# Kernel optimization log

Measured on AMD Instinct MI355X. Metric: run time of the kernel, lower is better.

The kernel has to match this reference:

```python
import jax, jax.numpy as jnp
import numpy as np

N = 10000          # nodes
E = 640000         # edges (avg degree 64)
D_EMB = 32
D_FEAT = 8
D = 256            # node_encoding
LAYERS = 3         # graph_layers
FLOW_ITERS = 10
COST_C = 1.0       # square cost: c*x^2, inv_derivative(y) = y/(2c)


def setup_inputs() -> dict:
    key = jax.random.key(0)
    ks = jax.random.split(key, 20)

    def gn(k, shape):
        return jax.random.normal(k, shape, jnp.float32) / np.sqrt(shape[0]).astype(np.float32)

    return dict(
        node_features=jax.random.normal(ks[0], (N, D_FEAT), jnp.float32),
        node_embeddings=jax.random.normal(ks[1], (N, D_EMB), jnp.float32),
        demands=jax.random.normal(ks[2], (N, 1), jnp.float32),
        edge_src=jnp.sort(jax.random.randint(ks[3], (E,), 0, N, jnp.int32)),
        edge_dst=jax.random.randint(ks[4], (E,), 0, N, jnp.int32),
        W_enc=gn(ks[5], (D_EMB + D_FEAT, D)), b_enc=jnp.zeros((D,), jnp.float32),
        W_agg_in=gn(ks[6], (D, D)), W_agg_out=gn(ks[7], (D, D)), b_agg=jnp.zeros((D,), jnp.float32),
        W_z=gn(ks[8], (D, D)), U_z=gn(ks[9], (D, D)), b_z=jnp.zeros((D,), jnp.float32),
        W_r=gn(ks[10], (D, D)), U_r=gn(ks[11], (D, D)), b_r=jnp.zeros((D,), jnp.float32),
        W_h=gn(ks[12], (D, D)), U_h=gn(ks[13], (D, D)), b_h=jnp.zeros((D,), jnp.float32),
        W_dec=gn(ks[14], (D, N)), b_dec=jnp.zeros((N,), jnp.float32),
        W_d1=gn(ks[15], (D, D)), b_d1=jnp.zeros((D,), jnp.float32),
        W_d2=gn(ks[16], (D, 1)), b_d2=jnp.zeros((1,), jnp.float32),
    )


def _segment_softmax(vals, seg, num):
    # tf.sparse.softmax: softmax over the nonzero entries of each row
    m = jax.ops.segment_max(vals, seg, num_segments=num, indices_are_sorted=True)
    e = jnp.exp(vals - m[seg])
    s = jax.ops.segment_sum(e, seg, num_segments=num, indices_are_sorted=True)
    return e / s[seg]


def reference(node_features, node_embeddings, demands, edge_src, edge_dst,
              W_enc, b_enc, W_agg_in, W_agg_out, b_agg,
              W_z, U_z, b_z, W_r, U_r, b_r, W_h, U_h, b_h,
              W_dec, b_dec, W_d1, b_d1, W_d2, b_d2):
    n = node_features.shape[0]
    # node encoder (MLP, no hidden, relu)
    h = jax.nn.relu(jnp.concatenate([node_embeddings, node_features], axis=1) @ W_enc + b_enc)
    # graph layers: sparse neighborhood aggregation + GRU state update
    for _ in range(LAYERS):
        t = h @ W_agg_in                                   # [N, D]
        agg = jax.ops.segment_sum(t[edge_dst], edge_src,    # gather neighbors, scatter-add by row
                                  num_segments=n, indices_are_sorted=True)
        nxt = jnp.tanh(agg @ W_agg_out + b_agg)
        z = jax.nn.sigmoid(nxt @ W_z + h @ U_z + b_z)
        r = jax.nn.sigmoid(nxt @ W_r + h @ U_r + b_r)
        cand = jnp.tanh(nxt @ W_h + (r * h) @ U_h + b_h)
        h = z * h + (1.0 - z) * cand
    # decoder -> dense [N, N] edge weights, masked by adjacency, sparse row softmax
    pred = h @ W_dec + b_dec                                # [N, N]
    logits = pred[edge_src, edge_dst]                       # [E]
    w = _segment_softmax(logits, edge_src, n)               # flow_weight_pred values
    # sparse min-cost-flow: proportional flow iterations
    d = demands[:, 0]
    flow = jnp.zeros_like(w)
    for _ in range(FLOW_ITERS):
        inflow = jax.ops.segment_sum(flow, edge_dst, num_segments=n)
        adj_in = jax.nn.relu(inflow - d)                    # flow available to push out of each node
        flow = w * adj_in[edge_src]
    flow_cost = jnp.sum(COST_C * flow * flow)
    # dual decoder (hidden [D] relu, linear head)
    dual = jax.nn.relu(h @ W_d1 + b_d1) @ W_d2 + b_d2       # [N, 1]
    dv = dual[:, 0]
    dual_diff = dv[edge_src] - dv[edge_dst]                 # (dual_i - dual_j) on edges only
    dual_flows = jax.nn.relu(dual_diff / (2.0 * COST_C))    # relu(inv_derivative)
    dual_cost = jnp.sum(COST_C * dual_flows * dual_flows - dual_flows * dual_diff) - jnp.sum(dv * d)
    loss = flow_cost - dual_cost
    return loss, flow
```

## Files before the change

### kernel.cpp

```cpp
#include <hip/hip_runtime.h>
#include <hip/hip_bf16.h>
#include <math.h>

#define N_NODES 10000
#define N_EDGES 640000
#define DDIM 256
#define NBLK_E 2500

typedef long long i64;

__device__ __forceinline__ float sigmoidf_(float x) { return 1.0f / (1.0f + expf(-x)); }

__global__ __launch_bounds__(256) void encode_kernel(
    const float* __restrict__ feat, const float* __restrict__ emb,
    const float* __restrict__ W, const float* __restrict__ b, float* __restrict__ h)
{
    const int n = blockIdx.x;
    const int t = threadIdx.x;
    __shared__ float in_s[40];
    if (t < 32) in_s[t] = emb[(i64)n * 32 + t];
    else if (t < 40) in_s[t] = feat[(i64)n * 8 + (t - 32)];
    __syncthreads();
    float acc = b[t];
#pragma unroll
    for (int k = 0; k < 40; ++k) acc += in_s[k] * W[k * DDIM + t];
    h[(i64)n * DDIM + t] = fmaxf(acc, 0.0f);
}

enum { EPI_NONE = 0, EPI_TANH, EPI_SIGM, EPI_RH, EPI_HOUT, EPI_RELU };

template<int EPI, bool DUAL>
__global__ __launch_bounds__(256) void gemm_epi(
    const float* __restrict__ A1, const float* __restrict__ W1,
    const float* __restrict__ A2, const float* __restrict__ W2,
    const float* __restrict__ bias,
    const float* __restrict__ haux, const float* __restrict__ zaux,
    float* __restrict__ C)
{
    __shared__ __align__(16) float As[16][68];
    __shared__ __align__(16) float Bs[16][64];
    const int tid = threadIdx.x;
    const int tx = tid & 15;
    const int ty = tid >> 4;
    const int brow = blockIdx.x * 64;
    const int bcol = blockIdx.y * 64;

    const int lrow = tid >> 2;
    const int lk4  = (tid & 3) << 2;
    const int wkrow = tid >> 4;
    const int wcol4 = (tid & 15) << 2;

    const int arow = brow + lrow;
    const bool arow_ok = (arow < N_NODES);
    const i64 aoff = (i64)(arow_ok ? arow : 0) * DDIM;

    float acc[4][4] = {{0.f,0.f,0.f,0.f},{0.f,0.f,0.f,0.f},{0.f,0.f,0.f,0.f},{0.f,0.f,0.f,0.f}};

    for (int pass = 0; pass < (DUAL ? 2 : 1); ++pass) {
        const float* Ap = (pass ? A2 : A1) + aoff;
        const float* Wp = (pass ? W2 : W1);
        for (int k0 = 0; k0 < DDIM; k0 += 16) {
            float4 av = arow_ok ? *(const float4*)(Ap + k0 + lk4) : make_float4(0.f,0.f,0.f,0.f);
            float4 wv = *(const float4*)(Wp + (i64)(k0 + wkrow) * DDIM + bcol + wcol4);
            __syncthreads();
            As[lk4+0][lrow] = av.x; As[lk4+1][lrow] = av.y;
            As[lk4+2][lrow] = av.z; As[lk4+3][lrow] = av.w;
            *(float4*)&Bs[wkrow][wcol4] = wv;
            __syncthreads();
#pragma unroll
            for (int k = 0; k < 16; ++k) {
                float4 a = *(const float4*)&As[k][ty << 2];
                float4 b = *(const float4*)&Bs[k][tx << 2];
                acc[0][0] += a.x*b.x; acc[0][1] += a.x*b.y; acc[0][2] += a.x*b.z; acc[0][3] += a.x*b.w;
                acc[1][0] += a.y*b.x; acc[1][1] += a.y*b.y; acc[1][2] += a.y*b.z; acc[1][3] += a.y*b.w;
                acc[2][0] += a.z*b.x; acc[2][1] += a.z*b.y; acc[2][2] += a.z*b.z; acc[2][3] += a.z*b.w;
                acc[3][0] += a.w*b.x; acc[3][1] += a.w*b.y; acc[3][2] += a.w*b.z; acc[3][3] += a.w*b.w;
            }
        }
    }

#pragma unroll
    for (int i = 0; i < 4; ++i) {
        const int r = brow + (ty << 2) + i;
        if (r < N_NODES) {
#pragma unroll
            for (int j = 0; j < 4; ++j) {
                const int c = bcol + (tx << 2) + j;
                const i64 idx = (i64)r * DDIM + c;
                float v = acc[i][j];
                float out;
                if constexpr (EPI == EPI_NONE)      out = v;
                else if constexpr (EPI == EPI_TANH) out = tanhf(v + bias[c]);
                else if constexpr (EPI == EPI_SIGM) out = sigmoidf_(v + bias[c]);
                else if constexpr (EPI == EPI_RH)   out = sigmoidf_(v + bias[c]) * haux[idx];
                else if constexpr (EPI == EPI_HOUT) {
                    float cand = tanhf(v + bias[c]);
                    float zz = zaux[idx];
                    out = zz * haux[idx] + (1.0f - zz) * cand;
                } else                               out = fmaxf(v + bias[c], 0.0f);
                C[idx] = out;
            }
        }
    }
}

__global__ __launch_bounds__(256) void agg_kernel(
    const float* __restrict__ t, const int* __restrict__ dst, const int* __restrict__ rp,
    float* __restrict__ agg)
{
    const int n = blockIdx.x;
    const int d = threadIdx.x;
    const int s = rp[n], e = rp[n + 1];
    float a0 = 0.f, a1 = 0.f, a2 = 0.f, a3 = 0.f;
    int i = s;
    for (; i + 4 <= e; i += 4) {
        int d0 = dst[i], d1 = dst[i+1], d2 = dst[i+2], d3 = dst[i+3];
        a0 += t[(i64)d0 * DDIM + d];
        a1 += t[(i64)d1 * DDIM + d];
        a2 += t[(i64)d2 * DDIM + d];
        a3 += t[(i64)d3 * DDIM + d];
    }
    for (; i < e; ++i) a0 += t[(i64)dst[i] * DDIM + d];
    agg[(i64)n * DDIM + d] = (a0 + a1) + (a2 + a3);
}

__global__ __launch_bounds__(256) void transpose_kernel(
    const float* __restrict__ Wd, float* __restrict__ wdt)
{
    __shared__ float tile[32][33];
    const int bx = blockIdx.x;
    const int by = blockIdx.y;
    const int tx = threadIdx.x & 31, ty = threadIdx.x >> 5;
#pragma unroll
    for (int j = 0; j < 4; ++j) {
        int k = by * 32 + ty + j * 8;
        int nc = bx * 32 + tx;
        if (nc < N_NODES) tile[ty + j * 8][tx] = Wd[(i64)k * N_NODES + nc];
    }
    __syncthreads();
#pragma unroll
    for (int j = 0; j < 4; ++j) {
        int nr = bx * 32 + ty + j * 8;
        int k = by * 32 + tx;
        if (nr < N_NODES) wdt[(i64)nr * DDIM + k] = tile[tx][ty + j * 8];
    }
}

__global__ __launch_bounds__(256) void logits_softmax_kernel(
    const float* __restrict__ h, const float* __restrict__ wdt,
    const float* __restrict__ b_dec, const int* __restrict__ dst,
    const int* __restrict__ rp, float* __restrict__ w)
{
    const int n = blockIdx.x;
    const int s = rp[n], e = rp[n + 1];
    const int tid = threadIdx.x;
    const int lane = tid & 63, wv = tid >> 6;
    __shared__ __align__(16) float hs[256];
    __shared__ float sred[8];
    hs[tid] = h[(i64)n * DDIM + tid];
    __syncthreads();
    float4 hv = ((const float4*)hs)[lane];
    for (int i = s + wv; i < e; i += 4) {
        const int dd = dst[i];
        float4 a = *(const float4*)(wdt + (i64)dd * DDIM + (lane << 2));
        float p = a.x*hv.x + a.y*hv.y + a.z*hv.z + a.w*hv.w;
#pragma unroll
        for (int o = 32; o; o >>= 1) p += __shfl_down(p, o);
        if (lane == 0) w[i] = p + b_dec[dd];
    }
    __syncthreads();
    if (e <= s) return;
    float m = -INFINITY;
    for (int i = s + tid; i < e; i += 256) m = fmaxf(m, w[i]);
#pragma unroll
    for (int o = 32; o; o >>= 1) m = fmaxf(m, __shfl_down(m, o));
    if (lane == 0) sred[wv] = m;
    __syncthreads();
    m = fmaxf(fmaxf(sred[0], sred[1]), fmaxf(sred[2], sred[3]));
    float ss = 0.f;
    for (int i = s + tid; i < e; i += 256) { float ev = expf(w[i] - m); w[i] = ev; ss += ev; }
#pragma unroll
    for (int o = 32; o; o >>= 1) ss += __shfl_down(ss, o);
    if (lane == 0) sred[4 + wv] = ss;
    __syncthreads();
    ss = (sred[4] + sred[5]) + (sred[6] + sred[7]);
    float inv = 1.0f / ss;
    for (int i = s + tid; i < e; i += 256) w[i] *= inv;
}

__global__ void zero_misc_kernel(int* __restrict__ cnt, float* __restrict__ red) {
    int i = blockIdx.x * 256 + threadIdx.x;
    if (i < N_NODES) cnt[i] = 0;
    if (i < 8) red[i] = 0.0f;
}

__global__ void rowptr_kernel(const int* __restrict__ key, int* __restrict__ rp) {
    int n = blockIdx.x * 256 + threadIdx.x;
    if (n > N_NODES) return;
    int lo = 0, hi = N_EDGES;
    while (lo < hi) { int mid = (lo + hi) >> 1; if (key[mid] < n) lo = mid + 1; else hi = mid; }
    rp[n] = lo;
}

__global__ void hist_kernel(const int* __restrict__ dst, int* __restrict__ cnt) {
    int e = blockIdx.x * 256 + threadIdx.x;
    atomicAdd(&cnt[dst[e]], 1);
}

__global__ __launch_bounds__(256) void scan_kernel(int* __restrict__ cnt, int* __restrict__ rp) {
    __shared__ int part[256];
    const int t = threadIdx.x;
    const int chunk = (N_NODES + 255) / 256;
    int b = t * chunk, en = min(b + chunk, N_NODES);
    int s = 0;
    for (int i = b; i < en; ++i) s += cnt[i];
    part[t] = s;
    __syncthreads();
    for (int o = 1; o < 256; o <<= 1) {
        int v = (t >= o) ? part[t - o] : 0;
        __syncthreads();
        part[t] += v;
        __syncthreads();
    }
    int base = (t == 0) ? 0 : part[t - 1];
    for (int i = b; i < en; ++i) { rp[i] = base; base += cnt[i]; cnt[i] = 0; }
    if (t == 255) rp[N_NODES] = part[255];
}

__global__ void scatter_kernel(const int* __restrict__ src, const int* __restrict__ dst,
                               const float* __restrict__ w, const int* __restrict__ rp_d,
                               int* __restrict__ cnt, int* __restrict__ sp, float* __restrict__ wp)
{
    int e = blockIdx.x * 256 + threadIdx.x;
    int dd = dst[e];
    int pos = rp_d[dd] + atomicAdd(&cnt[dd], 1);
    sp[pos] = src[e];
    wp[pos] = w[e];
}

__global__ void init_adj_kernel(const float* __restrict__ dem, float* __restrict__ adjA) {
    int n = blockIdx.x * 256 + threadIdx.x;
    if (n < N_NODES) adjA[n] = fmaxf(-dem[n], 0.0f);
}

__global__ __launch_bounds__(256) void flow_iter_kernel(
    const float* __restrict__ wp, const int* __restrict__ sp, const int* __restrict__ rp_d,
    const float* __restrict__ adj_old, const float* __restrict__ dem, float* __restrict__ adj_new)
{
    const int n = blockIdx.x * 4 + (threadIdx.x >> 6);
    if (n >= N_NODES) return;
    const int lane = threadIdx.x & 63;
    const int s = rp_d[n], e = rp_d[n + 1];
    float acc = 0.f;
    for (int i = s + lane; i < e; i += 64) acc += wp[i] * adj_old[sp[i]];
#pragma unroll
    for (int o = 32; o; o >>= 1) acc += __shfl_down(acc, o);
    if (lane == 0) adj_new[n] = fmaxf(acc - dem[n], 0.0f);
}

__global__ __launch_bounds__(256) void flow_out_kernel(
    const float* __restrict__ w, const int* __restrict__ src, const float* __restrict__ adj,
    float* __restrict__ out_flow, float* __restrict__ red)
{
    __shared__ float sred[4];
    int e = blockIdx.x * 256 + threadIdx.x;
    float f = w[e] * adj[src[e]];
    out_flow[e] = f;
    float p = f * f;
#pragma unroll
    for (int o = 32; o; o >>= 1) p += __shfl_down(p, o);
    int lane = threadIdx.x & 63, wv = threadIdx.x >> 6;
    if (lane == 0) sred[wv] = p;
    __syncthreads();
    if (threadIdx.x == 0) atomicAdd(&red[0], (sred[0] + sred[1]) + (sred[2] + sred[3]));
}

__global__ __launch_bounds__(256) void dv_kernel(
    const float* __restrict__ t2, const float* __restrict__ Wd2, const float* __restrict__ bd2,
    const float* __restrict__ dem, float* __restrict__ dv, float* __restrict__ red)
{
    __shared__ float sred[4];
    const int n = blockIdx.x * 4 + (threadIdx.x >> 6);
    const int lane = threadIdx.x & 63, wv = threadIdx.x >> 6;
    float contrib = 0.0f;
    if (n < N_NODES) {
        float4 a = *(const float4*)(t2 + (i64)n * DDIM + (lane << 2));
        float4 b = *(const float4*)(Wd2 + (lane << 2));
        float p = a.x*b.x + a.y*b.y + a.z*b.z + a.w*b.w;
#pragma unroll
        for (int o = 32; o; o >>= 1) p += __shfl_down(p, o);
        if (lane == 0) {
            float v = p + bd2[0];
            dv[n] = v;
            contrib = v * dem[n];
        }
    }
    if (lane == 0) sred[wv] = contrib;
    __syncthreads();
    if (threadIdx.x == 0) atomicAdd(&red[2], (sred[0] + sred[1]) + (sred[2] + sred[3]));
}

__global__ __launch_bounds__(256) void dual_edge_kernel(
    const float* __restrict__ dv, const int* __restrict__ src, const int* __restrict__ dst,
    float* __restrict__ red)
{
    __shared__ float sred[4];
    int e = blockIdx.x * 256 + threadIdx.x;
    float df = dv[src[e]] - dv[dst[e]];
    float f = fmaxf(df * 0.5f, 0.0f);
    float val = f * f - f * df;
#pragma unroll
    for (int o = 32; o; o >>= 1) val += __shfl_down(val, o);
    int lane = threadIdx.x & 63, wv = threadIdx.x >> 6;
    if (lane == 0) sred[wv] = val;
    __syncthreads();
    if (threadIdx.x == 0) atomicAdd(&red[1], (sred[0] + sred[1]) + (sred[2] + sred[3]));
}

__global__ void finalize_kernel(const float* __restrict__ red, float* __restrict__ out) {
    out[0] = red[0] - red[1] + red[2];
}

extern "C" void kernel_launch(void* const* d_in, const int* in_sizes, int n_in,
                              void* d_out, int out_size, void* d_ws, size_t ws_size,
                              hipStream_t stream) {
    (void)in_sizes; (void)n_in; (void)out_size; (void)ws_size;
    const float* feat   = (const float*)d_in[0];
    const float* emb    = (const float*)d_in[1];
    const float* dem    = (const float*)d_in[2];
    const int*   e_src  = (const int*)d_in[3];
    const int*   e_dst  = (const int*)d_in[4];
    const float* W_enc  = (const float*)d_in[5];
    const float* b_enc  = (const float*)d_in[6];
    const float* W_ai   = (const float*)d_in[7];
    const float* W_ao   = (const float*)d_in[8];
    const float* b_agg  = (const float*)d_in[9];
    const float* W_z    = (const float*)d_in[10];
    const float* U_z    = (const float*)d_in[11];
    const float* b_z    = (const float*)d_in[12];
    const float* W_r    = (const float*)d_in[13];
    const float* U_r    = (const float*)d_in[14];
    const float* b_r    = (const float*)d_in[15];
    const float* W_h    = (const float*)d_in[16];
    const float* U_h    = (const float*)d_in[17];
    const float* b_h    = (const float*)d_in[18];
    const float* W_dec  = (const float*)d_in[19];
    const float* b_dec  = (const float*)d_in[20];
    const float* W_d1   = (const float*)d_in[21];
    const float* b_d1   = (const float*)d_in[22];
    const float* W_d2   = (const float*)d_in[23];
    const float* b_d2   = (const float*)d_in[24];

    float* ws = (float*)d_ws;
    const size_t F = (size_t)N_NODES * DDIM;
    float* h    = ws;
    float* t    = ws + F;
    float* agg  = ws + 2 * F;
    float* nxt  = ws + 3 * F;
    float* wbuf = ws + 4 * F;
    float* wp   = wbuf + N_EDGES;
    int*   sp   = (int*)(wp + N_EDGES);
    float* adjA = (float*)(sp + N_EDGES);
    float* adjB = adjA + N_NODES;
    float* dv   = adjB + N_NODES;
    int*   rp_s = (int*)(dv + N_NODES);
    int*   rp_d = rp_s + (N_NODES + 1);
    int*   cnt  = rp_d + (N_NODES + 1);
    float* red  = (float*)(cnt + N_NODES);
    float* zb = t;
    float* rh = agg;
    float* wdt = agg;

    const dim3 g_gemm(157, 4);

    zero_misc_kernel<<<40, 256, 0, stream>>>(cnt, red);
    encode_kernel<<<N_NODES, 256, 0, stream>>>(feat, emb, W_enc, b_enc, h);
    rowptr_kernel<<<40, 256, 0, stream>>>(e_src, rp_s);

    for (int L = 0; L < 3; ++L) {
        gemm_epi<EPI_NONE, false><<<g_gemm, 256, 0, stream>>>(h, W_ai, nullptr, nullptr, nullptr, nullptr, nullptr, t);
        agg_kernel<<<N_NODES, 256, 0, stream>>>(t, e_dst, rp_s, agg);
        gemm_epi<EPI_TANH, false><<<g_gemm, 256, 0, stream>>>(agg, W_ao, nullptr, nullptr, b_agg, nullptr, nullptr, nxt);
        gemm_epi<EPI_SIGM, true><<<g_gemm, 256, 0, stream>>>(nxt, W_z, h, U_z, b_z, nullptr, nullptr, zb);
        gemm_epi<EPI_RH, true><<<g_gemm, 256, 0, stream>>>(nxt, W_r, h, U_r, b_r, h, nullptr, rh);
        gemm_epi<EPI_HOUT, true><<<g_gemm, 256, 0, stream>>>(nxt, W_h, rh, U_h, b_h, h, zb, h);
    }

    transpose_kernel<<<dim3(313, 8), 256, 0, stream>>>(W_dec, wdt);
    logits_softmax_kernel<<<N_NODES, 256, 0, stream>>>(h, wdt, b_dec, e_dst, rp_s, wbuf);

    hist_kernel<<<NBLK_E, 256, 0, stream>>>(e_dst, cnt);
    scan_kernel<<<1, 256, 0, stream>>>(cnt, rp_d);
    scatter_kernel<<<NBLK_E, 256, 0, stream>>>(e_src, e_dst, wbuf, rp_d, cnt, sp, wp);

    init_adj_kernel<<<40, 256, 0, stream>>>(dem, adjA);
    float* aold = adjA; float* anew = adjB;
    for (int it = 0; it < 9; ++it) {
        flow_iter_kernel<<<2500, 256, 0, stream>>>(wp, sp, rp_d, aold, dem, anew);
        float* tmp = aold; aold = anew; anew = tmp;
    }
    flow_out_kernel<<<NBLK_E, 256, 0, stream>>>(wbuf, e_src, aold, (float*)d_out + 1, red);

    gemm_epi<EPI_RELU, false><<<g_gemm, 256, 0, stream>>>(h, W_d1, nullptr, nullptr, b_d1, nullptr, nullptr, t);
    dv_kernel<<<2500, 256, 0, stream>>>(t, W_d2, b_d2, dem, dv, red);
    dual_edge_kernel<<<NBLK_E, 256, 0, stream>>>(dv, e_src, e_dst, red);
    finalize_kernel<<<1, 1, 0, stream>>>(red, (float*)d_out);
}
```

Baseline: 1.389 ms.

## Replace fp32 SIMT GEMMs with split-bf16 MFMA GEMMs for dense layers

```diff
diff --git a/kernel.cpp b/kernel.cpp
--- a/kernel.cpp
+++ b/kernel.cpp
@@ -8,8 +8,19 @@
 #define NBLK_E 2500
 
 typedef long long i64;
+typedef __attribute__((ext_vector_type(8))) short short8;
+typedef __attribute__((ext_vector_type(4))) float f32x4;
 
 __device__ __forceinline__ float sigmoidf_(float x) { return 1.0f / (1.0f + expf(-x)); }
+__device__ __forceinline__ short bf16_hi(float f, float& hf) {
+    __hip_bfloat16 h = __float2bfloat16(f);
+    hf = __bfloat162float(h);
+    return __builtin_bit_cast(short, h);
+}
+__device__ __forceinline__ short bf16_of(float f) {
+    __hip_bfloat16 h = __float2bfloat16(f);
+    return __builtin_bit_cast(short, h);
+}
 
 __global__ __launch_bounds__(256) void encode_kernel(
     const float* __restrict__ feat, const float* __restrict__ emb,
@@ -27,78 +38,120 @@
     h[(i64)n * DDIM + t] = fmaxf(acc, 0.0f);
 }
 
+struct Wsrc { const float* s[9]; };
+
+__global__ __launch_bounds__(256) void conv_w_kernel(Wsrc wsrc, short* __restrict__ wt)
+{
+    const int m = blockIdx.y;
+    const float* __restrict__ src = wsrc.s[m];
+    short* dh = wt + (i64)m * 131072;
+    short* dl = dh + 65536;
+    const int e = blockIdx.x * 256 + threadIdx.x;
+    const int c = e >> 8, k = e & 255;
+    const float f = src[k * 256 + c];
+    float hf;
+    const short hb = bf16_hi(f, hf);
+    dh[(i64)c * 256 + k] = hb;
+    dl[(i64)c * 256 + k] = bf16_of(f - hf);
+}
+
 enum { EPI_NONE = 0, EPI_TANH, EPI_SIGM, EPI_RH, EPI_HOUT, EPI_RELU };
 
+__device__ __forceinline__ void load_cvt_frag(const float* __restrict__ p, bool ok,
+                                              short8& hi, short8& lo)
+{
+    f32x4 v0 = {}, v1 = {};
+    if (ok) { v0 = *(const f32x4*)p; v1 = *(const f32x4*)(p + 4); }
+#pragma unroll
+    for (int j = 0; j < 4; ++j) {
+        float h0f, h1f;
+        hi[j]     = bf16_hi(v0[j], h0f);
+        hi[j + 4] = bf16_hi(v1[j], h1f);
+        lo[j]     = bf16_of(v0[j] - h0f);
+        lo[j + 4] = bf16_of(v1[j] - h1f);
+    }
+}
+
 template<int EPI, bool DUAL>
-__global__ __launch_bounds__(256) void gemm_epi(
-    const float* __restrict__ A1, const float* __restrict__ W1,
-    const float* __restrict__ A2, const float* __restrict__ W2,
+__global__ __launch_bounds__(256) void gemm_mfma(
+    const float* __restrict__ A1, const short* __restrict__ W1h, const short* __restrict__ W1l,
+    const float* __restrict__ A2, const short* __restrict__ W2h, const short* __restrict__ W2l,
     const float* __restrict__ bias,
     const float* __restrict__ haux, const float* __restrict__ zaux,
     float* __restrict__ C)
 {
-    __shared__ __align__(16) float As[16][68];
-    __shared__ __align__(16) float Bs[16][64];
     const int tid = threadIdx.x;
-    const int tx = tid & 15;
-    const int ty = tid >> 4;
-    const int brow = blockIdx.x * 64;
-    const int bcol = blockIdx.y * 64;
-
-    const int lrow = tid >> 2;
-    const int lk4  = (tid & 3) << 2;
-    const int wkrow = tid >> 4;
-    const int wcol4 = (tid & 15) << 2;
-
-    const int arow = brow + lrow;
-    const bool arow_ok = (arow < N_NODES);
-    const i64 aoff = (i64)(arow_ok ? arow : 0) * DDIM;
-
-    float acc[4][4] = {{0.f,0.f,0.f,0.f},{0.f,0.f,0.f,0.f},{0.f,0.f,0.f,0.f},{0.f,0.f,0.f,0.f}};
+    const int w = tid >> 6, lane = tid & 63;
+    const int lr = lane & 15, g = lane >> 4;
+    const int brow = blockIdx.x * 64 + (w >> 1) * 32;
+    const int bcol = blockIdx.y * 64 + (w & 1) * 32;
+
+    const int r0 = brow + lr, r1 = brow + 16 + lr;
+    const bool ok0 = r0 < N_NODES, ok1 = r1 < N_NODES;
+    const i64 wcoff0 = (i64)(bcol + lr) * 256 + 8 * g;
+    const i64 wcoff1 = (i64)(bcol + 16 + lr) * 256 + 8 * g;
+
+    f32x4 acc[2][2] = {};
 
     for (int pass = 0; pass < (DUAL ? 2 : 1); ++pass) {
-        const float* Ap = (pass ? A2 : A1) + aoff;
-        const float* Wp = (pass ? W2 : W1);
-        for (int k0 = 0; k0 < DDIM; k0 += 16) {
-            float4 av = arow_ok ? *(const float4*)(Ap + k0 + lk4) : make_float4(0.f,0.f,0.f,0.f);
-            float4 wv = *(const float4*)(Wp + (i64)(k0 + wkrow) * DDIM + bcol + wcol4);
-            __syncthreads();
-            As[lk4+0][lrow] = av.x; As[lk4+1][lrow] = av.y;
-            As[lk4+2][lrow] = av.z; As[lk4+3][lrow] = av.w;
-            *(float4*)&Bs[wkrow][wcol4] = wv;
-            __syncthreads();
-#pragma unroll
-            for (int k = 0; k < 16; ++k) {
-                float4 a = *(const float4*)&As[k][ty << 2];
-                float4 b = *(const float4*)&Bs[k][tx << 2];
-                acc[0][0] += a.x*b.x; acc[0][1] += a.x*b.y; acc[0][2] += a.x*b.z; acc[0][3] += a.x*b.w;
-                acc[1][0] += a.y*b.x; acc[1][1] += a.y*b.y; acc[1][2] += a.y*b.z; acc[1][3] += a.y*b.w;
-                acc[2][0] += a.z*b.x; acc[2][1] += a.z*b.y; acc[2][2] += a.z*b.z; acc[2][3] += a.z*b.w;
-                acc[3][0] += a.w*b.x; acc[3][1] += a.w*b.y; acc[3][2] += a.w*b.z; acc[3][3] += a.w*b.w;
-            }
+        const float* __restrict__ A  = pass ? A2 : A1;
+        const short* __restrict__ Wh = pass ? W2h : W1h;
+        const short* __restrict__ Wl = pass ? W2l : W1l;
+        const float* a0p = A + (i64)r0 * DDIM + 8 * g;
+        const float* a1p = A + (i64)r1 * DDIM + 8 * g;
+#pragma unroll 2
+        for (int k0 = 0; k0 < DDIM; k0 += 32) {
+            short8 a0h, a0l, a1h, a1l;
+            load_cvt_frag(a0p + k0, ok0, a0h, a0l);
+            load_cvt_frag(a1p + k0, ok1, a1h, a1l);
+            short8 b0h = *(const short8*)(Wh + wcoff0 + k0);
+            short8 b0l = *(const short8*)(Wl + wcoff0 + k0);
+            short8 b1h = *(const short8*)(Wh + wcoff1 + k0);
+            short8 b1l = *(const short8*)(Wl + wcoff1 + k0);
+
+            acc[0][0] = __builtin_amdgcn_mfma_f32_16x16x32_bf16(a0h, b0h, acc[0][0], 0, 0, 0);
+            acc[0][0] = __builtin_amdgcn_mfma_f32_16x16x32_bf16(a0h, b0l, acc[0][0], 0, 0, 0);
+            acc[0][0] = __builtin_amdgcn_mfma_f32_16x16x32_bf16(a0l, b0h, acc[0][0], 0, 0, 0);
+
+            acc[0][1] = __builtin_amdgcn_mfma_f32_16x16x32_bf16(a0h, b1h, acc[0][1], 0, 0, 0);
+            acc[0][1] = __builtin_amdgcn_mfma_f32_16x16x32_bf16(a0h, b1l, acc[0][1], 0, 0, 0);
+            acc[0][1] = __builtin_amdgcn_mfma_f32_16x16x32_bf16(a0l, b1h, acc[0][1], 0, 0, 0);
+
+            acc[1][0] = __builtin_amdgcn_mfma_f32_16x16x32_bf16(a1h, b0h, acc[1][0], 0, 0, 0);
+            acc[1][0] = __builtin_amdgcn_mfma_f32_16x16x32_bf16(a1h, b0l, acc[1][0], 0, 0, 0);
+            acc[1][0] = __builtin_amdgcn_mfma_f32_16x16x32_bf16(a1l, b0h, acc[1][0], 0, 0, 0);
+
+            acc[1][1] = __builtin_amdgcn_mfma_f32_16x16x32_bf16(a1h, b1h, acc[1][1], 0, 0, 0);
+            acc[1][1] = __builtin_amdgcn_mfma_f32_16x16x32_bf16(a1h, b1l, acc[1][1], 0, 0, 0);
+            acc[1][1] = __builtin_amdgcn_mfma_f32_16x16x32_bf16(a1l, b1h, acc[1][1], 0, 0, 0);
         }
     }
 
 #pragma unroll
-    for (int i = 0; i < 4; ++i) {
-        const int r = brow + (ty << 2) + i;
-        if (r < N_NODES) {
-#pragma unroll
-            for (int j = 0; j < 4; ++j) {
-                const int c = bcol + (tx << 2) + j;
-                const i64 idx = (i64)r * DDIM + c;
-                float v = acc[i][j];
-                float out;
-                if constexpr (EPI == EPI_NONE)      out = v;
-                else if constexpr (EPI == EPI_TANH) out = tanhf(v + bias[c]);
-                else if constexpr (EPI == EPI_SIGM) out = sigmoidf_(v + bias[c]);
-                else if constexpr (EPI == EPI_RH)   out = sigmoidf_(v + bias[c]) * haux[idx];
-                else if constexpr (EPI == EPI_HOUT) {
-                    float cand = tanhf(v + bias[c]);
-                    float zz = zaux[idx];
-                    out = zz * haux[idx] + (1.0f - zz) * cand;
-                } else                               out = fmaxf(v + bias[c], 0.0f);
-                C[idx] = out;
+    for (int ct = 0; ct < 2; ++ct) {
+        const int c = bcol + ct * 16 + lr;
+        float b_c = 0.0f;
+        if constexpr (EPI != EPI_NONE) b_c = bias[c];
+#pragma unroll
+        for (int rt = 0; rt < 2; ++rt) {
+#pragma unroll
+            for (int q = 0; q < 4; ++q) {
+                const int r = brow + rt * 16 + 4 * g + q;
+                if (r < N_NODES) {
+                    const i64 idx = (i64)r * DDIM + c;
+                    const float v = acc[rt][ct][q];
+                    float out;
+                    if constexpr (EPI == EPI_NONE)      out = v;
+                    else if constexpr (EPI == EPI_TANH) out = tanhf(v + b_c);
+                    else if constexpr (EPI == EPI_SIGM) out = sigmoidf_(v + b_c);
+                    else if constexpr (EPI == EPI_RH)   out = sigmoidf_(v + b_c) * haux[idx];
+                    else if constexpr (EPI == EPI_HOUT) {
+                        float cand = tanhf(v + b_c);
+                        float zz = zaux[idx];
+                        out = zz * haux[idx] + (1.0f - zz) * cand;
+                    } else                               out = fmaxf(v + b_c, 0.0f);
+                    C[idx] = out;
+                }
             }
         }
     }
@@ -367,23 +420,40 @@
     int*   rp_d = rp_s + (N_NODES + 1);
     int*   cnt  = rp_d + (N_NODES + 1);
     float* red  = (float*)(cnt + N_NODES);
+    short* wt   = (short*)(red + 8);
     float* zb = t;
     float* rh = agg;
     float* wdt = agg;
 
+    short* ai_h = wt + 0*131072; short* ai_l = ai_h + 65536;
+    short* ao_h = wt + 1*131072; short* ao_l = ao_h + 65536;
+    short* z_h  = wt + 2*131072; short* z_l  = z_h  + 65536;
+    short* uz_h = wt + 3*131072; short* uz_l = uz_h + 65536;
+    short* r_h  = wt + 4*131072; short* r_l  = r_h  + 65536;
+    short* ur_h = wt + 5*131072; short* ur_l = ur_h + 65536;
+    short* wh_h = wt + 6*131072; short* wh_l = wh_h + 65536;
+    short* uh_h = wt + 7*131072; short* uh_l = uh_h + 65536;
+    short* d1_h = wt + 8*131072; short* d1_l = d1_h + 65536;
+
     const dim3 g_gemm(157, 4);
 
+    Wsrc wsrc;
+    wsrc.s[0] = W_ai; wsrc.s[1] = W_ao; wsrc.s[2] = W_z; wsrc.s[3] = U_z;
+    wsrc.s[4] = W_r;  wsrc.s[5] = U_r;  wsrc.s[6] = W_h; wsrc.s[7] = U_h;
+    wsrc.s[8] = W_d1;
+
     zero_misc_kernel<<<40, 256, 0, stream>>>(cnt, red);
+    conv_w_kernel<<<dim3(256, 9), 256, 0, stream>>>(wsrc, wt);
     encode_kernel<<<N_NODES, 256, 0, stream>>>(feat, emb, W_enc, b_enc, h);
     rowptr_kernel<<<40, 256, 0, stream>>>(e_src, rp_s);
 
     for (int L = 0; L < 3; ++L) {
-        gemm_epi<EPI_NONE, false><<<g_gemm, 256, 0, stream>>>(h, W_ai, nullptr, nullptr, nullptr, nullptr, nullptr, t);
+        gemm_mfma<EPI_NONE, false><<<g_gemm, 256, 0, stream>>>(h, ai_h, ai_l, nullptr, nullptr, nullptr, nullptr, nullptr, nullptr, t);
         agg_kernel<<<N_NODES, 256, 0, stream>>>(t, e_dst, rp_s, agg);
-        gemm_epi<EPI_TANH, false><<<g_gemm, 256, 0, stream>>>(agg, W_ao, nullptr, nullptr, b_agg, nullptr, nullptr, nxt);
-        gemm_epi<EPI_SIGM, true><<<g_gemm, 256, 0, stream>>>(nxt, W_z, h, U_z, b_z, nullptr, nullptr, zb);
-        gemm_epi<EPI_RH, true><<<g_gemm, 256, 0, stream>>>(nxt, W_r, h, U_r, b_r, h, nullptr, rh);
-        gemm_epi<EPI_HOUT, true><<<g_gemm, 256, 0, stream>>>(nxt, W_h, rh, U_h, b_h, h, zb, h);
+        gemm_mfma<EPI_TANH, false><<<g_gemm, 256, 0, stream>>>(agg, ao_h, ao_l, nullptr, nullptr, nullptr, b_agg, nullptr, nullptr, nxt);
+        gemm_mfma<EPI_SIGM, true><<<g_gemm, 256, 0, stream>>>(nxt, z_h, z_l, h, uz_h, uz_l, b_z, nullptr, nullptr, zb);
+        gemm_mfma<EPI_RH, true><<<g_gemm, 256, 0, stream>>>(nxt, r_h, r_l, h, ur_h, ur_l, b_r, h, nullptr, rh);
+        gemm_mfma<EPI_HOUT, true><<<g_gemm, 256, 0, stream>>>(nxt, wh_h, wh_l, rh, uh_h, uh_l, b_h, h, zb, h);
     }
 
     transpose_kernel<<<dim3(313, 8), 256, 0, stream>>>(W_dec, wdt);
@@ -401,7 +471,7 @@
     }
     flow_out_kernel<<<NBLK_E, 256, 0, stream>>>(wbuf, e_src, aold, (float*)d_out + 1, red);
 
-    gemm_epi<EPI_RELU, false><<<g_gemm, 256, 0, stream>>>(h, W_d1, nullptr, nullptr, b_d1, nullptr, nullptr, t);
+    gemm_mfma<EPI_RELU, false><<<g_gemm, 256, 0, stream>>>(h, d1_h, d1_l, nullptr, nullptr, nullptr, b_d1, nullptr, nullptr, t);
     dv_kernel<<<2500, 256, 0, stream>>>(t, W_d2, b_d2, dem, dv, red);
     dual_edge_kernel<<<NBLK_E, 256, 0, stream>>>(dv, e_src, e_dst, red);
     finalize_kernel<<<1, 1, 0, stream>>>(red, (float*)d_out);
```

Result: faster. 1.361 ms (-2.0%).
